# Kernel optimization log

Measured on AMD Instinct MI355X. Metric: run time of the kernel, lower is better.

Reference implementation:

```python
import jax, jax.numpy as jnp
import numpy as np

B, S, E, H = 2, 2048, 1024, 16
DH = E // H


def setup_inputs() -> dict:
    key = jax.random.key(0)
    ks = jax.random.split(key, 9)
    inp = {
        "query": jax.random.normal(ks[0], (B, S, E), dtype=jnp.float32),
        "key": jax.random.normal(ks[1], (B, S, E), dtype=jnp.float32),
        "value": jax.random.normal(ks[2], (B, S, E), dtype=jnp.float32),
        # causal mask: True means "masked out" (masked_fill semantics)
        "mask": jnp.broadcast_to(
            jnp.triu(jnp.ones((S, S), dtype=bool), k=1)[None, None], (B, 1, S, S)
        ),
        # learned parameters (nn.Linear weight is [out, in]; y = x @ W.T + b)
        "Wq": jax.random.normal(ks[3], (E, E), dtype=jnp.float32) / np.sqrt(E),
        "Wk": jax.random.normal(ks[4], (E, E), dtype=jnp.float32) / np.sqrt(E),
        "Wv": jax.random.normal(ks[5], (E, E), dtype=jnp.float32) / np.sqrt(E),
        "Wo": jax.random.normal(ks[6], (E, E), dtype=jnp.float32) / np.sqrt(E),
        "bo": jax.random.normal(ks[7], (E,), dtype=jnp.float32) * 0.01,
    }
    return inp


def reference(query, key, value, mask, Wq, Wk, Wv, Wo, bo):
    # projections (no bias for q/k/v)
    Q = query @ Wq.T  # [B,S,E]
    K = key @ Wk.T
    V = value @ Wv.T
    # split heads: [B,S,E] -> [B,H,S,Dh]
    Q = Q.reshape(B, S, H, DH).transpose(0, 2, 1, 3)
    K = K.reshape(B, S, H, DH).transpose(0, 2, 1, 3)
    V = V.reshape(B, S, H, DH).transpose(0, 2, 1, 3)
    scale = 1.0 / np.sqrt(DH).astype(np.float32)
    scores = jnp.einsum("bhqd,bhkd->bhqk", Q, K) * scale  # [B,H,S,S]
    scores = jnp.where(mask, -jnp.inf, scores)
    attn = jax.nn.softmax(scores, axis=-1)
    # dropout(p=0.2) is identity in eval mode
    out = jnp.einsum("bhqk,bhkd->bhqd", attn, V)  # [B,H,S,Dh]
    out = out.transpose(0, 2, 1, 3).reshape(B, S, E)
    return out @ Wo.T + bo
```

## Files before the change

### kernel.cpp

```cpp
#include <hip/hip_runtime.h>
#include <hip/hip_bf16.h>
#include <stdint.h>

#define Bb 2
#define Ss 2048
#define Ee 1024
#define Hh 16
#define Dh 64

typedef __bf16 bf16_t;
typedef __attribute__((ext_vector_type(8))) __bf16 bf16x8;
typedef __attribute__((ext_vector_type(4))) __bf16 bf16x4;
typedef __attribute__((ext_vector_type(4))) float f32x4;

#define QSCALE_LOG2E 0.18033688011112042f

__device__ inline void gload_lds16(const void* g, void* l) {
  __builtin_amdgcn_global_load_lds((__attribute__((address_space(1))) void*)g,
                                   (__attribute__((address_space(3))) void*)l,
                                   16, 0, 0);
}

struct Cvt7 {
  const float* s[7];
  bf16_t* d[7];
  int n8[7];
};

__global__ __launch_bounds__(256) void cvt_f32_bf16(Cvt7 c) {
  int gid = blockIdx.x * 256 + threadIdx.x;
#pragma unroll
  for (int j = 0; j < 7; ++j) {
    if (gid < c.n8[j]) {
      const float* s = c.s[j] + (size_t)gid * 8;
      const f32x4 lo = *(const f32x4*)s;
      const f32x4 hi = *(const f32x4*)(s + 4);
      bf16x8 v;
      v[0] = (bf16_t)lo[0]; v[1] = (bf16_t)lo[1];
      v[2] = (bf16_t)lo[2]; v[3] = (bf16_t)lo[3];
      v[4] = (bf16_t)hi[0]; v[5] = (bf16_t)hi[1];
      v[6] = (bf16_t)hi[2]; v[7] = (bf16_t)hi[3];
      *(bf16x8*)(c.d[j] + (size_t)gid * 8) = v;
      return;
    }
    gid -= c.n8[j];
  }
}

template <int ROWS>
__device__ __forceinline__ void stage_bf16(const bf16_t* __restrict__ src,
                                           int ldk, int k0, bf16_t* lds,
                                           int wave, int lane) {
  const int srow = lane >> 3, sslot = lane & 7;
#pragma unroll
  for (int r = 0; r < ROWS / 32; ++r) {
    const int chunk = wave + r * 4;
    const int row = chunk * 8 + srow;
    const int k16 = sslot ^ (row & 7);
    gload_lds16(src + (size_t)row * ldk + k0 + k16 * 8, lds + chunk * 512);
  }
}

__device__ __forceinline__ void mfma_tile_128(const bf16_t* As,
                                              const bf16_t* Bs, int wr, int wc,
                                              int lr, int lg, f32x4 acc[4][4]) {
  const char* a_base = (const char*)As;
  const char* b_base = (const char*)Bs;
#pragma unroll
  for (int kk = 0; kk < 2; ++kk) {
    bf16x8 af[4], bfr[4];
#pragma unroll
    for (int x = 0; x < 4; ++x) {
      const int arow = wr * 64 + x * 16 + lr;
      af[x] = *(const bf16x8*)(a_base + ((arow * 128 + kk * 64 + lg * 16) ^
                                         ((arow & 7) << 4)));
      const int brow = wc * 64 + x * 16 + lr;
      bfr[x] = *(const bf16x8*)(b_base + ((brow * 128 + kk * 64 + lg * 16) ^
                                          ((brow & 7) << 4)));
    }
#pragma unroll
    for (int mi = 0; mi < 4; ++mi)
#pragma unroll
      for (int ni = 0; ni < 4; ++ni)
        acc[mi][ni] = __builtin_amdgcn_mfma_f32_16x16x32_bf16(
            af[mi], bfr[ni], acc[mi][ni], 0, 0, 0);
  }
}

__global__ __launch_bounds__(256) void qkv_proj(
    const bf16_t* __restrict__ Aq, const bf16_t* __restrict__ Ak,
    const bf16_t* __restrict__ Av, const bf16_t* __restrict__ Wq,
    const bf16_t* __restrict__ Wk, const bf16_t* __restrict__ Wv,
    bf16_t* __restrict__ Cq, bf16_t* __restrict__ Ck,
    bf16_t* __restrict__ Cv) {
  __shared__ bf16_t As[2][128 * 64];
  __shared__ bf16_t Bs[2][128 * 64];
  const int z = blockIdx.z;
  const bf16_t* A = (z == 0) ? Aq : (z == 1) ? Ak : Av;
  const bf16_t* W = (z == 0) ? Wq : (z == 1) ? Wk : Wv;
  bf16_t* C = (z == 0) ? Cq : (z == 1) ? Ck : Cv;

  const int wg = blockIdx.y * 8 + blockIdx.x;
  const int virt = (wg & 7) * 32 + (wg >> 3);
  const int n0 = (virt & 7) * 128, m0 = (virt >> 3) * 128;

  const int tid = threadIdx.x;
  const int lane = tid & 63, wave = tid >> 6;
  const int wr = wave >> 1, wc = wave & 1;
  const int lr = lane & 15, lg = lane >> 4;

  const bf16_t* Arow = A + (size_t)m0 * Ee;
  const bf16_t* Wrow = W + (size_t)n0 * Ee;

  f32x4 acc[4][4] = {};

  stage_bf16<128>(Arow, Ee, 0, As[0], wave, lane);
  stage_bf16<128>(Wrow, Ee, 0, Bs[0], wave, lane);
  asm volatile("s_waitcnt vmcnt(0)" ::: "memory");
  __syncthreads();

  int cur = 0;
  for (int t = 0; t < Ee / 64; ++t) {
    if (t + 1 < Ee / 64) {
      stage_bf16<128>(Arow, Ee, (t + 1) * 64, As[cur ^ 1], wave, lane);
      stage_bf16<128>(Wrow, Ee, (t + 1) * 64, Bs[cur ^ 1], wave, lane);
    }
    mfma_tile_128(As[cur], Bs[cur], wr, wc, lr, lg, acc);
    asm volatile("s_waitcnt vmcnt(0)" ::: "memory");
    __syncthreads();
    cur ^= 1;
  }

#pragma unroll
  for (int mi = 0; mi < 4; ++mi) {
#pragma unroll
    for (int i = 0; i < 4; ++i) {
      const int m = m0 + wr * 64 + mi * 16 + lg * 4 + i;
#pragma unroll
      for (int ni = 0; ni < 4; ++ni) {
        const int n = n0 + wc * 64 + ni * 16 + lr;
        float v = acc[mi][ni][i];
        if (z == 0) v *= QSCALE_LOG2E;
        const int b = m >> 11, s = m & (Ss - 1);
        const int h = n >> 6, d = n & 63;
        if (z != 2)
          C[(((size_t)(b * Hh + h)) * Ss + s) * Dh + d] = (bf16_t)v;
        else
          C[(((size_t)(b * Hh + h)) * Dh + d) * Ss + s] = (bf16_t)v;
      }
    }
  }
}

__global__ __launch_bounds__(256) void out_gemm(const bf16_t* __restrict__ A,
                                                const bf16_t* __restrict__ W,
                                                const float* __restrict__ bias,
                                                float* __restrict__ C) {
  __shared__ bf16_t As[2][128 * 64];
  __shared__ bf16_t Bs[2][64 * 64];
  const int wg = blockIdx.y * 16 + blockIdx.x;
  const int virt = (wg & 7) * 64 + (wg >> 3);
  const int n0 = (virt & 15) * 64, m0 = (virt >> 4) * 128;

  const int tid = threadIdx.x;
  const int lane = tid & 63, wave = tid >> 6;
  const int lr = lane & 15, lg = lane >> 4;

  const bf16_t* Arow = A + (size_t)m0 * Ee;
  const bf16_t* Wrow = W + (size_t)n0 * Ee;

  f32x4 acc[2][4] = {};

  stage_bf16<128>(Arow, Ee, 0, As[0], wave, lane);
  stage_bf16<64>(Wrow, Ee, 0, Bs[0], wave, lane);
  asm volatile("s_waitcnt vmcnt(0)" ::: "memory");
  __syncthreads();

  int cur = 0;
  for (int t = 0; t < Ee / 64; ++t) {
    if (t + 1 < Ee / 64) {
      stage_bf16<128>(Arow, Ee, (t + 1) * 64, As[cur ^ 1], wave, lane);
      stage_bf16<64>(Wrow, Ee, (t + 1) * 64, Bs[cur ^ 1], wave, lane);
    }

    const char* a_base = (const char*)As[cur];
    const char* b_base = (const char*)Bs[cur];
#pragma unroll
    for (int kk = 0; kk < 2; ++kk) {
      bf16x8 af[2], bfr[4];
#pragma unroll
      for (int x = 0; x < 2; ++x) {
        const int arow = wave * 32 + x * 16 + lr;
        af[x] = *(const bf16x8*)(a_base + ((arow * 128 + kk * 64 + lg * 16) ^
                                           ((arow & 7) << 4)));
      }
#pragma unroll
      for (int ni = 0; ni < 4; ++ni) {
        const int brow = ni * 16 + lr;
        bfr[ni] = *(const bf16x8*)(b_base + ((brow * 128 + kk * 64 + lg * 16) ^
                                             ((brow & 7) << 4)));
      }
#pragma unroll
      for (int mi = 0; mi < 2; ++mi)
#pragma unroll
        for (int ni = 0; ni < 4; ++ni)
          acc[mi][ni] = __builtin_amdgcn_mfma_f32_16x16x32_bf16(
              af[mi], bfr[ni], acc[mi][ni], 0, 0, 0);
    }
    asm volatile("s_waitcnt vmcnt(0)" ::: "memory");
    __syncthreads();
    cur ^= 1;
  }

#pragma unroll
  for (int mi = 0; mi < 2; ++mi) {
#pragma unroll
    for (int i = 0; i < 4; ++i) {
      const int m = m0 + wave * 32 + mi * 16 + lg * 4 + i;
#pragma unroll
      for (int ni = 0; ni < 4; ++ni) {
        const int n = n0 + ni * 16 + lr;
        C[(size_t)m * Ee + n] = acc[mi][ni][i] + bias[n];
      }
    }
  }
}


__device__ __forceinline__ void attn_stage(const bf16_t* Kh, const bf16_t* Vh,
                                           int kv0, int wave, int lane,
                                           bf16_t* KsBuf, bf16_t* VsBuf) {
#pragma unroll
  for (int r = 0; r < 4; ++r) {
    const int c = wave + r * 4;
    const int krow = c * 8 + (lane >> 3);
    const int ks = (lane & 7) ^ (krow & 7);
    gload_lds16(Kh + (size_t)(kv0 + krow) * Dh + ks * 8, KsBuf + c * 512);
    const int vrow = c * 4 + (lane >> 4);
    const int vs = (lane & 15) ^ (vrow & 7);
    gload_lds16(Vh + (size_t)vrow * Ss + kv0 + vs * 8, VsBuf + c * 512);
  }
}

template <int NI, bool MASKED>
__device__ __forceinline__ void attn_tile_compute(
    int kv0, int qw, int lane, char* pb, const char* kb, const char* vb,
    const bf16x8 aq[2], float& m_run, float& l_run, f32x4 oacc[4]) {
  const int lr = lane & 15, lg = lane >> 4;

  f32x4 sc[NI];
#pragma unroll
  for (int ni = 0; ni < NI; ++ni) {
    const int krow = ni * 16 + lr;
    const bf16x8 ak0 =
        *(const bf16x8*)(kb + ((krow * 128 + lg * 16) ^ ((krow & 7) << 4)));
    const bf16x8 ak1 = *(const bf16x8*)(kb + ((krow * 128 + 64 + lg * 16) ^
                                              ((krow & 7) << 4)));
    f32x4 z = {0.f, 0.f, 0.f, 0.f};
    z = __builtin_amdgcn_mfma_f32_16x16x32_bf16(ak0, aq[0], z, 0, 0, 0);
    z = __builtin_amdgcn_mfma_f32_16x16x32_bf16(ak1, aq[1], z, 0, 0, 0);
    sc[ni] = z;
  }

  if (MASKED) {
    const int q_rel = qw + lr - kv0;
#pragma unroll
    for (int ni = 0; ni < NI; ++ni)
#pragma unroll
      for (int i = 0; i < 4; ++i)
        if (ni * 16 + lg * 4 + i > q_rel) sc[ni][i] = -1e30f;
  }

  f32x4 vm = sc[0];
#pragma unroll
  for (int ni = 1; ni < NI; ++ni)
#pragma unroll
    for (int i = 0; i < 4; ++i) vm[i] = fmaxf(vm[i], sc[ni][i]);
  float rm = fmaxf(fmaxf(vm[0], vm[1]), fmaxf(vm[2], vm[3]));
  rm = fmaxf(rm, __shfl_xor(rm, 16));
  rm = fmaxf(rm, __shfl_xor(rm, 32));

  const float mo = m_run;
  const float mn = fmaxf(mo, rm);
  const float corr = __builtin_amdgcn_exp2f(mo - mn);
  m_run = mn;

  f32x4 vs = {0.f, 0.f, 0.f, 0.f};
#pragma unroll
  for (int ni = 0; ni < NI; ++ni) {
    bf16x4 w;
#pragma unroll
    for (int i = 0; i < 4; ++i) {
      const float p = __builtin_amdgcn_exp2f(sc[ni][i] - mn);
      vs[i] += p;
      w[i] = (bf16_t)p;
    }
    *(bf16x4*)(pb + ((lr * 256 + ni * 32 + lg * 8) ^ ((lr & 7) << 4))) = w;
  }
  float rs = (vs[0] + vs[1]) + (vs[2] + vs[3]);
  rs += __shfl_xor(rs, 16);
  rs += __shfl_xor(rs, 32);
  l_run = l_run * corr + rs;

#pragma unroll
  for (int i = 0; i < 4; ++i) {
    const float ci = __shfl(corr, (lane & 48) | (lg * 4 + i));
#pragma unroll
    for (int di = 0; di < 4; ++di) oacc[di][i] *= ci;
  }

#pragma unroll
  for (int kk = 0; kk < NI / 2; ++kk) {
    const bf16x8 pa = *(const bf16x8*)(pb + ((lr * 256 + kk * 64 + lg * 16) ^
                                             ((lr & 7) << 4)));
#pragma unroll
    for (int di = 0; di < 4; ++di) {
      const int vrow = di * 16 + lr;
      const bf16x8 bv = *(const bf16x8*)(vb + ((vrow * 256 + kk * 64 +
                                                lg * 16) ^
                                               ((vrow & 7) << 4)));
      oacc[di] =
          __builtin_amdgcn_mfma_f32_16x16x32_bf16(pa, bv, oacc[di], 0, 0, 0);
    }
  }
}

__device__ __forceinline__ void flash_qtile(int qt, const bf16_t* Qh,
                                            const bf16_t* Kh, const bf16_t* Vh,
                                            bf16_t* AO_row, int wave, int lane,
                                            bf16_t* Ks, bf16_t* Vs,
                                            bf16_t* PsW) {
  const int lr = lane & 15, lg = lane >> 4;
  const int qw = qt * 64 + wave * 16;

  bf16x8 aq[2];
#pragma unroll
  for (int kd = 0; kd < 2; ++kd)
    aq[kd] = *(const bf16x8*)(Qh + (size_t)(qw + lr) * Dh + kd * 32 + lg * 8);

  f32x4 oacc[4] = {};
  float m_run = -1e30f, l_run = 0.f;
  char* pb = (char*)PsW;

  const int nt = (qt + 2) >> 1;
  attn_stage(Kh, Vh, 0, wave, lane, Ks, Vs);
  asm volatile("s_waitcnt vmcnt(0)" ::: "memory");
  __syncthreads();

  for (int t = 0; t < nt; ++t) {
    const int cur = t & 1;
    if (t + 1 < nt)
      attn_stage(Kh, Vh, (t + 1) * 128, wave, lane, Ks + (cur ^ 1) * 8192,
                 Vs + (cur ^ 1) * 8192);
    const char* kb = (const char*)(Ks + cur * 8192);
    const char* vb = (const char*)(Vs + cur * 8192);
    if (t < nt - 1)
      attn_tile_compute<8, false>(t * 128, qw, lane, pb, kb, vb, aq, m_run,
                                  l_run, oacc);
    else if ((qt & 1) == 0)
      attn_tile_compute<4, true>(t * 128, qw, lane, pb, kb, vb, aq, m_run,
                                 l_run, oacc);
    else
      attn_tile_compute<8, true>(t * 128, qw, lane, pb, kb, vb, aq, m_run,
                                 l_run, oacc);
    asm volatile("s_waitcnt vmcnt(0)" ::: "memory");
    __syncthreads();
  }

#pragma unroll
  for (int i = 0; i < 4; ++i) {
    const float li = __shfl(l_run, (lane & 48) | (lg * 4 + i));
    const float inv = 1.0f / li;
    const int s = qw + lg * 4 + i;
#pragma unroll
    for (int di = 0; di < 4; ++di) {
      const int d = di * 16 + lr;
      AO_row[(size_t)s * Ee + d] = (bf16_t)(oacc[di][i] * inv);
    }
  }
}

__global__ __launch_bounds__(256, 2) void attn_causal(
    const bf16_t* __restrict__ Qg, const bf16_t* __restrict__ Kg,
    const bf16_t* __restrict__ Vg, bf16_t* __restrict__ AO) {
  const int wg = blockIdx.y * 16 + blockIdx.x;
  const int virt = (wg & 7) * 64 + (wg >> 3);
  const int qx = virt & 15;
  const int bh = virt >> 4;

  const int tid = threadIdx.x;
  const int lane = tid & 63, wave = tid >> 6;

  const bf16_t* Qh = Qg + (size_t)bh * Ss * Dh;
  const bf16_t* Kh = Kg + (size_t)bh * Ss * Dh;
  const bf16_t* Vh = Vg + (size_t)bh * Dh * Ss;
  const int b = bh >> 4, h = bh & 15;
  bf16_t* AO_row = AO + (size_t)b * Ss * Ee + h * 64;

  __shared__ bf16_t Ks[2][128 * 64];
  __shared__ bf16_t Vs[2][64 * 128];
  __shared__ bf16_t Ps[4][16 * 128];

  const int qtA = qx;
  const int qtB = 31 - qx;
  flash_qtile(qtA, Qh, Kh, Vh, AO_row, wave, lane, Ks[0], Vs[0], Ps[wave]);
  flash_qtile(qtB, Qh, Kh, Vh, AO_row, wave, lane, Ks[0], Vs[0], Ps[wave]);
}

extern "C" void kernel_launch(void* const* d_in, const int* in_sizes, int n_in,
                              void* d_out, int out_size, void* d_ws,
                              size_t ws_size, hipStream_t stream) {
  const float* query = (const float*)d_in[0];
  const float* key = (const float*)d_in[1];
  const float* value = (const float*)d_in[2];
  const float* Wq = (const float*)d_in[4];
  const float* Wk = (const float*)d_in[5];
  const float* Wv = (const float*)d_in[6];
  const float* Wo = (const float*)d_in[7];
  const float* bo = (const float*)d_in[8];

  const size_t T = (size_t)Bb * Ss * Ee;
  const size_t WN = (size_t)Ee * Ee;
  bf16_t* qbf = (bf16_t*)d_ws;
  bf16_t* kbf = qbf + T;
  bf16_t* vbf = kbf + T;
  bf16_t* wqb = vbf + T;
  bf16_t* wkb = wqb + WN;
  bf16_t* wvb = wkb + WN;
  bf16_t* wob = wvb + WN;
  bf16_t* qws = wob + WN;
  bf16_t* kws = qws + T;
  bf16_t* vws = kws + T;
  bf16_t* aows = qbf;

  Cvt7 c;
  c.s[0] = query; c.d[0] = qbf; c.n8[0] = (int)(T / 8);
  c.s[1] = key;   c.d[1] = kbf; c.n8[1] = (int)(T / 8);
  c.s[2] = value; c.d[2] = vbf; c.n8[2] = (int)(T / 8);
  c.s[3] = Wq;    c.d[3] = wqb; c.n8[3] = (int)(WN / 8);
  c.s[4] = Wk;    c.d[4] = wkb; c.n8[4] = (int)(WN / 8);
  c.s[5] = Wv;    c.d[5] = wvb; c.n8[5] = (int)(WN / 8);
  c.s[6] = Wo;    c.d[6] = wob; c.n8[6] = (int)(WN / 8);
  const int total8 = (int)((3 * T + 4 * WN) / 8);

  dim3 blk(256);
  cvt_f32_bf16<<<dim3(total8 / 256), blk, 0, stream>>>(c);
  qkv_proj<<<dim3(Ee / 128, (Bb * Ss) / 128, 3), blk, 0, stream>>>(
      qbf, kbf, vbf, wqb, wkb, wvb, qws, kws, vws);
  attn_causal<<<dim3(16, Bb * Hh), blk, 0, stream>>>(qws, kws, vws, aows);
  out_gemm<<<dim3(Ee / 64, (Bb * Ss) / 128), blk, 0, stream>>>(
      aows, wob, bo, (float*)d_out);
}
```

Baseline: 132.0 us.

## Use partial vmcnt waits to keep two stages of loads in flight

The QKV projection GEMM, output projection GEMM and attention loop now wait on vmcnt with a nonzero count (8 or 6) instead of draining every outstanding load. The next tile's global-to-LDS loads stay in flight while the current tile is computed. In the GEMMs, the prefetch is issued two tiles ahead into the buffer just consumed, which needs an extra barrier after compute. The correctness of the counts depends on exactly how many load instructions each stage issues.

```diff
diff --git a/kernel.cpp b/kernel.cpp
--- a/kernel.cpp
+++ b/kernel.cpp
@@ -116,19 +116,22 @@
 
   stage_bf16<128>(Arow, Ee, 0, As[0], wave, lane);
   stage_bf16<128>(Wrow, Ee, 0, Bs[0], wave, lane);
-  asm volatile("s_waitcnt vmcnt(0)" ::: "memory");
-  __syncthreads();
-
-  int cur = 0;
-  for (int t = 0; t < Ee / 64; ++t) {
-    if (t + 1 < Ee / 64) {
-      stage_bf16<128>(Arow, Ee, (t + 1) * 64, As[cur ^ 1], wave, lane);
-      stage_bf16<128>(Wrow, Ee, (t + 1) * 64, Bs[cur ^ 1], wave, lane);
-    }
+  stage_bf16<128>(Arow, Ee, 64, As[1], wave, lane);
+  stage_bf16<128>(Wrow, Ee, 64, Bs[1], wave, lane);
+
+  for (int t = 0; t < 16; ++t) {
+    const int cur = t & 1;
+    if (t < 15)
+      asm volatile("s_waitcnt vmcnt(8)" ::: "memory");
+    else
+      asm volatile("s_waitcnt vmcnt(0)" ::: "memory");
+    __syncthreads();
     mfma_tile_128(As[cur], Bs[cur], wr, wc, lr, lg, acc);
-    asm volatile("s_waitcnt vmcnt(0)" ::: "memory");
-    __syncthreads();
-    cur ^= 1;
+    __syncthreads();
+    if (t + 2 < 16) {
+      stage_bf16<128>(Arow, Ee, (t + 2) * 64, As[cur], wave, lane);
+      stage_bf16<128>(Wrow, Ee, (t + 2) * 64, Bs[cur], wave, lane);
+    }
   }
 
 #pragma unroll
@@ -173,15 +176,16 @@
 
   stage_bf16<128>(Arow, Ee, 0, As[0], wave, lane);
   stage_bf16<64>(Wrow, Ee, 0, Bs[0], wave, lane);
-  asm volatile("s_waitcnt vmcnt(0)" ::: "memory");
-  __syncthreads();
-
-  int cur = 0;
-  for (int t = 0; t < Ee / 64; ++t) {
-    if (t + 1 < Ee / 64) {
-      stage_bf16<128>(Arow, Ee, (t + 1) * 64, As[cur ^ 1], wave, lane);
-      stage_bf16<64>(Wrow, Ee, (t + 1) * 64, Bs[cur ^ 1], wave, lane);
-    }
+  stage_bf16<128>(Arow, Ee, 64, As[1], wave, lane);
+  stage_bf16<64>(Wrow, Ee, 64, Bs[1], wave, lane);
+
+  for (int t = 0; t < 16; ++t) {
+    const int cur = t & 1;
+    if (t < 15)
+      asm volatile("s_waitcnt vmcnt(6)" ::: "memory");
+    else
+      asm volatile("s_waitcnt vmcnt(0)" ::: "memory");
+    __syncthreads();
 
     const char* a_base = (const char*)As[cur];
     const char* b_base = (const char*)Bs[cur];
@@ -207,9 +211,11 @@
           acc[mi][ni] = __builtin_amdgcn_mfma_f32_16x16x32_bf16(
               af[mi], bfr[ni], acc[mi][ni], 0, 0, 0);
     }
-    asm volatile("s_waitcnt vmcnt(0)" ::: "memory");
-    __syncthreads();
-    cur ^= 1;
+    __syncthreads();
+    if (t + 2 < 16) {
+      stage_bf16<128>(Arow, Ee, (t + 2) * 64, As[cur], wave, lane);
+      stage_bf16<64>(Wrow, Ee, (t + 2) * 64, Bs[cur], wave, lane);
+    }
   }
 
 #pragma unroll
@@ -344,14 +350,17 @@
 
   const int nt = (qt + 2) >> 1;
   attn_stage(Kh, Vh, 0, wave, lane, Ks, Vs);
-  asm volatile("s_waitcnt vmcnt(0)" ::: "memory");
-  __syncthreads();
 
   for (int t = 0; t < nt; ++t) {
     const int cur = t & 1;
-    if (t + 1 < nt)
+    if (t + 1 < nt) {
       attn_stage(Kh, Vh, (t + 1) * 128, wave, lane, Ks + (cur ^ 1) * 8192,
                  Vs + (cur ^ 1) * 8192);
+      asm volatile("s_waitcnt vmcnt(8)" ::: "memory");
+    } else {
+      asm volatile("s_waitcnt vmcnt(0)" ::: "memory");
+    }
+    __syncthreads();
     const char* kb = (const char*)(Ks + cur * 8192);
     const char* vb = (const char*)(Vs + cur * 8192);
     if (t < nt - 1)
@@ -363,7 +372,6 @@
     else
       attn_tile_compute<8, true>(t * 128, qw, lane, pb, kb, vb, aq, m_run,
                                  l_run, oacc);
-    asm volatile("s_waitcnt vmcnt(0)" ::: "memory");
     __syncthreads();
   }
 
```

Measured after the change: 117.9 us. -10.7%, faster.
